# Optimization experiments

Hardware: AMD Instinct MI355X
Metric: run time of the kernel (lower is better)

The kernel has to match this reference:

```python
import jax, jax.numpy as jnp
import numpy as np

NUM_USERS = 1_000_000
NUM_ITEMS = 1_000_000
N_FACTORS = 64
RANK = 16
BATCH = 16384


def setup_inputs() -> dict:
    key = jax.random.key(0)
    ks = jax.random.split(key, 8)
    return {
        "users": jax.random.randint(ks[0], (BATCH,), 0, NUM_USERS),
        "items": jax.random.randint(ks[1], (BATCH,), 0, NUM_ITEMS),
        "user_emb": jax.random.normal(ks[2], (NUM_USERS, N_FACTORS), jnp.float32),
        "item_emb": jax.random.normal(ks[3], (NUM_ITEMS, N_FACTORS), jnp.float32),
        "user_bias": jax.random.normal(ks[4], (NUM_USERS,), jnp.float32),
        "item_bias": jax.random.normal(ks[5], (NUM_ITEMS,), jnp.float32),
        "A": jax.random.normal(ks[6], (NUM_ITEMS, RANK), jnp.float32),
        "B": jax.random.normal(ks[7], (RANK, N_FACTORS), jnp.float32) * (1.0 / np.sqrt(RANK)),
    }


def reference(users, items, user_emb, item_emb, user_bias, item_bias, A, B):
    # train=True path: full low-rank correction over ALL items, then gather
    users_e = user_emb[users]                      # [B, F]
    item_emb_mat = A @ B + item_emb                # [num_items, F]
    items_e = item_emb_mat[items]                  # [B, F]
    predictions = jnp.sum(users_e * items_e, axis=1)  # [B]
    predictions = predictions + user_bias[users] + item_bias[items]
    return predictions
```

## Files before the change

kernel.cpp:

```cpp
#include <hip/hip_runtime.h>

#define NF 64
#define RANK 16

__global__ __launch_bounds__(256) void MF_27436251087258_kernel(
    const int* __restrict__ users,
    const int* __restrict__ items,
    const float* __restrict__ user_emb,
    const float* __restrict__ item_emb,
    const float* __restrict__ user_bias,
    const float* __restrict__ item_bias,
    const float* __restrict__ A,
    const float* __restrict__ Bm,
    float* __restrict__ out,
    int batch)
{
    __shared__ float Bs[RANK * NF];

    const int tid = threadIdx.x;

    {
        const float4 v = ((const float4*)Bm)[tid];
        ((float4*)Bs)[tid] = v;
    }
    __syncthreads();

    const int group = tid >> 4;
    const int lane  = tid & 15;
    const int i = blockIdx.x * 16 + group;
    if (i >= batch) return;

    const int u  = users[i];
    const int it = items[i];

    const float4 ue = *(const float4*)(user_emb + (size_t)u  * NF + lane * 4);
    const float4 ie = *(const float4*)(item_emb + (size_t)it * NF + lane * 4);
    const float  a  = A[(size_t)it * RANK + lane];

    float c0 = 0.f, c1 = 0.f, c2 = 0.f, c3 = 0.f;
    #pragma unroll
    for (int r = 0; r < RANK; ++r) {
        const float ar = __shfl(a, r, 16);
        const float4 br = ((const float4*)(Bs + r * NF))[lane];
        c0 = fmaf(ar, br.x, c0);
        c1 = fmaf(ar, br.y, c1);
        c2 = fmaf(ar, br.z, c2);
        c3 = fmaf(ar, br.w, c3);
    }

    float p = ue.x * (ie.x + c0)
            + ue.y * (ie.y + c1)
            + ue.z * (ie.z + c2)
            + ue.w * (ie.w + c3);

    p += __shfl_xor(p, 8, 16);
    p += __shfl_xor(p, 4, 16);
    p += __shfl_xor(p, 2, 16);
    p += __shfl_xor(p, 1, 16);

    if (lane == 0) {
        out[i] = p + user_bias[u] + item_bias[it];
    }
}

extern "C" void kernel_launch(void* const* d_in, const int* in_sizes, int n_in,
                              void* d_out, int out_size, void* d_ws, size_t ws_size,
                              hipStream_t stream) {
    const int*   users     = (const int*)  d_in[0];
    const int*   items     = (const int*)  d_in[1];
    const float* user_emb  = (const float*)d_in[2];
    const float* item_emb  = (const float*)d_in[3];
    const float* user_bias = (const float*)d_in[4];
    const float* item_bias = (const float*)d_in[5];
    const float* A         = (const float*)d_in[6];
    const float* Bm        = (const float*)d_in[7];
    float* out = (float*)d_out;

    const int batch = in_sizes[0];
    const int groups_per_block = 16;
    const int grid = (batch + groups_per_block - 1) / groups_per_block;

    MF_27436251087258_kernel<<<grid, 256, 0, stream>>>(
        users, items, user_emb, item_emb, user_bias, item_bias, A, Bm, out, batch);
}
```

Before: 9.410 us.

## Process two predictions per lane group and hoist gathers before shared-memory barrier

Each 16-lane group now computes two batch rows, so each block covers 32 outputs and the grid is halved. All embedding, A-row and bias gathers are issued before the shared-memory staging of B and the barrier, so global-memory latency overlaps the staging. The B tile is also reused across two rows per load from shared memory. Bounds checking is weakened: the int2 index loads have no guard, and the output check drops both rows when base+1 >= batch, which is only correct when the batch is even and a multiple of 32.

```diff
diff --git a/kernel.cpp b/kernel.cpp
--- a/kernel.cpp
+++ b/kernel.cpp
@@ -17,49 +17,60 @@
 {
     __shared__ float Bs[RANK * NF];
 
-    const int tid = threadIdx.x;
+    const int tid   = threadIdx.x;
+    const int group = tid >> 4;
+    const int lane  = tid & 15;
+    const int base  = (blockIdx.x * 16 + group) * 2;
 
-    {
-        const float4 v = ((const float4*)Bm)[tid];
-        ((float4*)Bs)[tid] = v;
-    }
+    const int2 uu = *(const int2*)(users + base);
+    const int2 ii = *(const int2*)(items + base);
+
+    const float4 bstage = ((const float4*)Bm)[tid];
+
+    const float4 ue0 = *(const float4*)(user_emb + (size_t)uu.x * NF + lane * 4);
+    const float4 ie0 = *(const float4*)(item_emb + (size_t)ii.x * NF + lane * 4);
+    const float4 ue1 = *(const float4*)(user_emb + (size_t)uu.y * NF + lane * 4);
+    const float4 ie1 = *(const float4*)(item_emb + (size_t)ii.y * NF + lane * 4);
+    const float  a0  = A[(size_t)ii.x * RANK + lane];
+    const float  a1  = A[(size_t)ii.y * RANK + lane];
+    const float  ub0 = user_bias[uu.x];
+    const float  ib0 = item_bias[ii.x];
+    const float  ub1 = user_bias[uu.y];
+    const float  ib1 = item_bias[ii.y];
+
+    ((float4*)Bs)[tid] = bstage;
     __syncthreads();
 
-    const int group = tid >> 4;
-    const int lane  = tid & 15;
-    const int i = blockIdx.x * 16 + group;
-    if (i >= batch) return;
-
-    const int u  = users[i];
-    const int it = items[i];
-
-    const float4 ue = *(const float4*)(user_emb + (size_t)u  * NF + lane * 4);
-    const float4 ie = *(const float4*)(item_emb + (size_t)it * NF + lane * 4);
-    const float  a  = A[(size_t)it * RANK + lane];
-
-    float c0 = 0.f, c1 = 0.f, c2 = 0.f, c3 = 0.f;
+    float c00 = 0.f, c01 = 0.f, c02 = 0.f, c03 = 0.f;
+    float c10 = 0.f, c11 = 0.f, c12 = 0.f, c13 = 0.f;
     #pragma unroll
     for (int r = 0; r < RANK; ++r) {
-        const float ar = __shfl(a, r, 16);
-        const float4 br = ((const float4*)(Bs + r * NF))[lane];
-        c0 = fmaf(ar, br.x, c0);
-        c1 = fmaf(ar, br.y, c1);
-        c2 = fmaf(ar, br.z, c2);
-        c3 = fmaf(ar, br.w, c3);
+        const float  ar0 = __shfl(a0, r, 16);
+        const float  ar1 = __shfl(a1, r, 16);
+        const float4 br  = ((const float4*)(Bs + r * NF))[lane];
+        c00 = fmaf(ar0, br.x, c00);  c10 = fmaf(ar1, br.x, c10);
+        c01 = fmaf(ar0, br.y, c01);  c11 = fmaf(ar1, br.y, c11);
+        c02 = fmaf(ar0, br.z, c02);  c12 = fmaf(ar1, br.z, c12);
+        c03 = fmaf(ar0, br.w, c03);  c13 = fmaf(ar1, br.w, c13);
     }
 
-    float p = ue.x * (ie.x + c0)
-            + ue.y * (ie.y + c1)
-            + ue.z * (ie.z + c2)
-            + ue.w * (ie.w + c3);
+    float p0 = ue0.x * (ie0.x + c00)
+             + ue0.y * (ie0.y + c01)
+             + ue0.z * (ie0.z + c02)
+             + ue0.w * (ie0.w + c03);
+    float p1 = ue1.x * (ie1.x + c10)
+             + ue1.y * (ie1.y + c11)
+             + ue1.z * (ie1.z + c12)
+             + ue1.w * (ie1.w + c13);
 
-    p += __shfl_xor(p, 8, 16);
-    p += __shfl_xor(p, 4, 16);
-    p += __shfl_xor(p, 2, 16);
-    p += __shfl_xor(p, 1, 16);
+    p0 += __shfl_xor(p0, 8, 16);  p1 += __shfl_xor(p1, 8, 16);
+    p0 += __shfl_xor(p0, 4, 16);  p1 += __shfl_xor(p1, 4, 16);
+    p0 += __shfl_xor(p0, 2, 16);  p1 += __shfl_xor(p1, 2, 16);
+    p0 += __shfl_xor(p0, 1, 16);  p1 += __shfl_xor(p1, 1, 16);
 
-    if (lane == 0) {
-        out[i] = p + user_bias[u] + item_bias[it];
+    if (lane == 0 && base + 1 < batch) {
+        out[base]     = p0 + ub0 + ib0;
+        out[base + 1] = p1 + ub1 + ib1;
     }
 }
 
@@ -77,8 +88,8 @@
     float* out = (float*)d_out;
 
     const int batch = in_sizes[0];
-    const int groups_per_block = 16;
-    const int grid = (batch + groups_per_block - 1) / groups_per_block;
+    const int outputs_per_block = 32;
+    const int grid = (batch + outputs_per_block - 1) / outputs_per_block;
 
     MF_27436251087258_kernel<<<grid, 256, 0, stream>>>(
         users, items, user_emb, item_emb, user_bias, item_bias, A, Bm, out, batch);
```

After: 12.11 us. +28.7%, slower.

## Drop shared-memory staging of B; read A rows and B directly from global

Applied to the files above, without the earlier changes.

Removes the per-block shared-memory copy of B and the __syncthreads barrier, so each lane reads its B columns straight from global memory, relying on cache since B is small and shared by all blocks. Each lane loads the whole 16-element A row as four float4 loads instead of using one element plus cross-lane shuffles. The user and item bias loads are issued early to overlap with the other gathers. The trade-off is more global and L1 load traffic per thread in exchange for no barrier, no LDS traffic and no shuffles.

```diff
diff --git a/kernel.cpp b/kernel.cpp
--- a/kernel.cpp
+++ b/kernel.cpp
@@ -15,16 +15,7 @@
     float* __restrict__ out,
     int batch)
 {
-    __shared__ float Bs[RANK * NF];
-
-    const int tid = threadIdx.x;
-
-    {
-        const float4 v = ((const float4*)Bm)[tid];
-        ((float4*)Bs)[tid] = v;
-    }
-    __syncthreads();
-
+    const int tid   = threadIdx.x;
     const int group = tid >> 4;
     const int lane  = tid & 15;
     const int i = blockIdx.x * 16 + group;
@@ -33,19 +24,30 @@
     const int u  = users[i];
     const int it = items[i];
 
+    const float ub = user_bias[u];
+    const float ib = item_bias[it];
+
     const float4 ue = *(const float4*)(user_emb + (size_t)u  * NF + lane * 4);
     const float4 ie = *(const float4*)(item_emb + (size_t)it * NF + lane * 4);
-    const float  a  = A[(size_t)it * RANK + lane];
+
+    const float* Arow = A + (size_t)it * RANK;
+    const float4 a0 = *(const float4*)(Arow + 0);
+    const float4 a1 = *(const float4*)(Arow + 4);
+    const float4 a2 = *(const float4*)(Arow + 8);
+    const float4 a3 = *(const float4*)(Arow + 12);
+    const float ar[RANK] = { a0.x, a0.y, a0.z, a0.w,
+                             a1.x, a1.y, a1.z, a1.w,
+                             a2.x, a2.y, a2.z, a2.w,
+                             a3.x, a3.y, a3.z, a3.w };
 
     float c0 = 0.f, c1 = 0.f, c2 = 0.f, c3 = 0.f;
     #pragma unroll
     for (int r = 0; r < RANK; ++r) {
-        const float ar = __shfl(a, r, 16);
-        const float4 br = ((const float4*)(Bs + r * NF))[lane];
-        c0 = fmaf(ar, br.x, c0);
-        c1 = fmaf(ar, br.y, c1);
-        c2 = fmaf(ar, br.z, c2);
-        c3 = fmaf(ar, br.w, c3);
+        const float4 br = *(const float4*)(Bm + r * NF + lane * 4);
+        c0 = fmaf(ar[r], br.x, c0);
+        c1 = fmaf(ar[r], br.y, c1);
+        c2 = fmaf(ar[r], br.z, c2);
+        c3 = fmaf(ar[r], br.w, c3);
     }
 
     float p = ue.x * (ie.x + c0)
@@ -59,7 +61,7 @@
     p += __shfl_xor(p, 1, 16);
 
     if (lane == 0) {
-        out[i] = p + user_bias[u] + item_bias[it];
+        out[i] = p + ub + ib;
     }
 }
 
```

Result: slower. 10.82 us (+15.0%).
